# Kernel tuning notes

Hardware: AMD Instinct MI355X
Metric: run time of the kernel (lower is better)

Reference implementation:

```python
import jax, jax.numpy as jnp
import numpy as np

N = 16384
C = 4        # in_channels
K = 16       # neighbors
H = 64       # mlp width


def setup_inputs() -> dict:
    key = jax.random.key(0)
    k0, k1, k2, k3, k4 = jax.random.split(key, 5)
    x = jax.random.normal(k0, (N, C), dtype=jnp.float32)
    # nn.Linear(2C, 64) and nn.Linear(64, 64): weight [out, in], bias [out]
    W1 = jax.random.normal(k1, (H, 2 * C), dtype=jnp.float32) * (1.0 / np.sqrt(2 * C))
    b1 = jax.random.normal(k2, (H,), dtype=jnp.float32) * 0.01
    W2 = jax.random.normal(k3, (H, H), dtype=jnp.float32) * (1.0 / np.sqrt(H))
    b2 = jax.random.normal(k4, (H,), dtype=jnp.float32) * 0.01
    return {"x": x, "W1": W1, "b1": b1, "W2": W2, "b2": b2}


def reference(x, W1, b1, W2, b2):
    # x: [N, C] single point cloud (torch code unsqueezes batch dim 0)
    xs = jax.lax.stop_gradient(x)  # knn indices computed under no_grad
    # pairwise = -||xi - xj||^2 = 2*xi.xj - ||xi||^2 - ||xj||^2
    xx = jnp.sum(xs * xs, axis=1)                      # [N]
    pairwise = 2.0 * (xs @ xs.T) - xx[:, None] - xx[None, :]  # [N, N]
    _, idx = jax.lax.top_k(pairwise, K)                # [N, K] (self included, dist 0 is max)
    neigh = x[idx]                                     # [N, K, C] gather
    center = jnp.broadcast_to(x[:, None, :], (x.shape[0], K, C))
    edge = jnp.concatenate([neigh - center, center], axis=-1)  # [N, K, 2C]
    h = jax.nn.relu(jnp.einsum('nkc,hc->nkh', edge, W1) + b1)
    h = jax.nn.relu(jnp.einsum('nkh,gh->nkg', h, W2) + b2)     # [N, K, H]
    out = jnp.mean(h, axis=1)                          # [N, H]
    return out[None]                                   # [1, N, H] matches torch output
```

## Files before the change

### kernel.cpp

```cpp
#include <hip/hip_runtime.h>
#include <math.h>

#define N_PTS 16384
#define K_NBR 16
#define H_DIM 64
#define TS    512
#define CAP   144

typedef unsigned long long u64;
typedef float v2f __attribute__((ext_vector_type(2)));

__device__ __forceinline__ int prefix_lt(u64 m) {
    return __builtin_amdgcn_mbcnt_hi((unsigned)(m >> 32),
           __builtin_amdgcn_mbcnt_lo((unsigned)m, 0));
}
__device__ __forceinline__ u64 mkkey(unsigned vbits, unsigned idx) {
    unsigned of = vbits ^ (unsigned)(((int)vbits >> 31) | 0x80000000);
    return ((u64)of << 32) | (unsigned)(~idx);
}
__device__ __forceinline__ unsigned keyidx(u64 k) { return ~(unsigned)k; }

__device__ __forceinline__ float readlane_f(float v, int l) {
    return __uint_as_float(__builtin_amdgcn_readlane(__float_as_uint(v), l));
}

__device__ __forceinline__ float wave_sort_f32(float v, int lane) {
#pragma unroll
    for (int k = 2; k <= 64; k <<= 1) {
#pragma unroll
        for (int j = k >> 1; j > 0; j >>= 1) {
            float o = __shfl_xor(v, j, 64);
            bool keep_min = (((lane & k) == 0) == ((lane & j) == 0));
            v = keep_min ? fminf(v, o) : fmaxf(v, o);
        }
    }
    return v;
}
__device__ __forceinline__ u64 wave_sort_u64(u64 v, int lane) {
#pragma unroll
    for (int k = 2; k <= 64; k <<= 1) {
#pragma unroll
        for (int j = k >> 1; j > 0; j >>= 1) {
            u64 o = __shfl_xor((unsigned long long)v, j, 64);
            bool keep_min = (((lane & k) == 0) == ((lane & j) == 0));
            u64 mn = (v < o) ? v : o;
            u64 mx = (v < o) ? o : v;
            v = keep_min ? mn : mx;
        }
    }
    return v;
}

__device__ __forceinline__ int wave_compact(uint2* buf, int cnt, float* tau,
                                            int lane) {
    float lm = -INFINITY;
    for (int s = lane; s < cnt; s += 64)
        lm = fmaxf(lm, __uint_as_float(buf[s].x));
    const float tv = readlane_f(wave_sort_f32(lm, lane), 48);
    int nc = 0;
    for (int s0 = 0; s0 < cnt; s0 += 64) {
        const int s = s0 + lane;
        uint2 e = make_uint2(0u, 0u);
        bool keep = false;
        if (s < cnt) { e = buf[s]; keep = (__uint_as_float(e.x) >= tv); }
        const u64 km = __ballot(keep);
        if (keep) buf[nc + prefix_lt(km)] = e;
        nc += (int)__popcll(km);
    }
    *tau = tv;
    return nc;
}

__global__ __launch_bounds__(256) void xx_kernel(const float4* __restrict__ x4,
                                                 float* __restrict__ xx) {
    int i = blockIdx.x * 256 + threadIdx.x;
    float4 v = x4[i];
    {
#pragma clang fp contract(off)
        float s0 = v.x * v.x;
        float s1 = v.y * v.y;
        float s2 = v.z * v.z;
        float s3 = v.w * v.w;
        xx[i] = ((s0 + s1) + s2) + s3;
    }
}

__global__ __launch_bounds__(256, 8) void knn_kernel(
        const float4* __restrict__ x4,
        const float* __restrict__ xx,
        int* __restrict__ knn) {
    __shared__ float xsc[4][TS];
    __shared__ float nxxs[TS];
    __shared__ uint2 buf[8][CAP];
    const int lane = threadIdx.x & 63;
    const int wave = threadIdx.x >> 6;
    const int row0 = blockIdx.x * 8 + wave * 2;

    float4 y[2]; float nxxi[2];
    uint2* bufr[2];
#pragma unroll
    for (int r = 0; r < 2; ++r) {
        const float4 t0 = x4[row0 + r];
        y[r] = make_float4(2.0f * t0.x, 2.0f * t0.y, 2.0f * t0.z, 2.0f * t0.w);
        nxxi[r] = -xx[row0 + r];
        bufr[r] = &buf[wave * 2 + r][0];
    }
    float tau[2]; int cnt[2];

    auto pair_p = [&](int e, int r) -> v2f {
        const v2f ax = *(const v2f*)&xsc[0][e];
        const v2f ay = *(const v2f*)&xsc[1][e];
        const v2f az = *(const v2f*)&xsc[2][e];
        const v2f aw = *(const v2f*)&xsc[3][e];
        const v2f nx = *(const v2f*)&nxxs[e];
        v2f acc = nx + (v2f){nxxi[r], nxxi[r]};
        acc = __builtin_elementwise_fma(ax, (v2f){y[r].x, y[r].x}, acc);
        acc = __builtin_elementwise_fma(ay, (v2f){y[r].y, y[r].y}, acc);
        acc = __builtin_elementwise_fma(az, (v2f){y[r].z, y[r].z}, acc);
        acc = __builtin_elementwise_fma(aw, (v2f){y[r].w, y[r].w}, acc);
        return acc;
    };

    for (int i = threadIdx.x; i < TS; i += 256) {
        const float4 v = x4[i];
        xsc[0][i] = v.x; xsc[1][i] = v.y; xsc[2][i] = v.z; xsc[3][i] = v.w;
        nxxs[i] = -xx[i];
    }
    __syncthreads();

    {
        const int e = 2 * lane;
#pragma unroll
        for (int r = 0; r < 2; ++r) {
            const v2f pp = pair_p(e, r);
            const float mx = fmaxf(pp.x, pp.y);
            tau[r] = readlane_f(wave_sort_f32(mx, lane), 48);
            const u64 ma = __ballot(pp.x >= tau[r]);
            const u64 mb = __ballot(pp.y >= tau[r]);
            const int ca = (int)__popcll(ma);
            if (pp.x >= tau[r])
                bufr[r][prefix_lt(ma)] =
                    make_uint2(__float_as_uint(pp.x), (unsigned)e);
            if (pp.y >= tau[r])
                bufr[r][ca + prefix_lt(mb)] =
                    make_uint2(__float_as_uint(pp.y), (unsigned)(e + 1));
            cnt[r] = ca + (int)__popcll(mb);
        }
    }

    auto do_iter = [&](int cbase) {
        const int e = (cbase & (TS - 1)) + 2 * lane;
        v2f pp[2]; u64 mm[2];
#pragma unroll
        for (int r = 0; r < 2; ++r) {
            pp[r] = pair_p(e, r);
            mm[r] = __ballot(fmaxf(pp[r].x, pp[r].y) > tau[r]);
        }
        if (mm[0] | mm[1]) {
#pragma unroll
            for (int r = 0; r < 2; ++r) {
                if (mm[r]) {
                    u64 ma = __ballot(pp[r].x > tau[r]);
                    u64 mb = __ballot(pp[r].y > tau[r]);
                    int add = (int)__popcll(ma) + (int)__popcll(mb);
                    if (cnt[r] + add > CAP) {
                        cnt[r] = wave_compact(bufr[r], cnt[r], &tau[r], lane);
                        ma = __ballot(pp[r].x > tau[r]);
                        mb = __ballot(pp[r].y > tau[r]);
                        add = (int)__popcll(ma) + (int)__popcll(mb);
                    }
                    const int ca = (int)__popcll(ma);
                    if (pp[r].x > tau[r])
                        bufr[r][cnt[r] + prefix_lt(ma)] =
                            make_uint2(__float_as_uint(pp[r].x),
                                       (unsigned)(cbase + 2 * lane));
                    if (pp[r].y > tau[r])
                        bufr[r][cnt[r] + ca + prefix_lt(mb)] =
                            make_uint2(__float_as_uint(pp[r].y),
                                       (unsigned)(cbase + 2 * lane + 1));
                    cnt[r] += add;
                }
            }
        }
    };

#pragma unroll
    for (int j = 1; j < TS / 128; ++j) do_iter(j * 128);

    for (int t = 1; t < N_PTS / TS; ++t) {
        const int base = t * TS;
        __syncthreads();
        for (int i = threadIdx.x; i < TS; i += 256) {
            const float4 v = x4[base + i];
            xsc[0][i] = v.x; xsc[1][i] = v.y; xsc[2][i] = v.z; xsc[3][i] = v.w;
            nxxs[i] = -xx[base + i];
        }
        __syncthreads();
#pragma unroll
        for (int j = 0; j < TS / 128; ++j) do_iter(base + j * 128);
    }

#pragma unroll
    for (int r = 0; r < 2; ++r) {
        const int c2 = wave_compact(bufr[r], cnt[r], &tau[r], lane);
        u64 key = 0;
        if (lane < c2) {
            const uint2 e = bufr[r][lane];
            key = mkkey(e.x, e.y);
        }
        key = wave_sort_u64(key, lane);
        if (lane >= 48)
            knn[(row0 + r) * K_NBR + (lane - 48)] = (int)keyidx(key);
    }
}

__global__ __launch_bounds__(256, 2) void mlp_kernel(
        const float4* __restrict__ x4,
        const int* __restrict__ knn,
        const float4* __restrict__ W2f4,
        const float* __restrict__ W1,
        const float* __restrict__ b1,
        const float* __restrict__ b2,
        float* __restrict__ out) {
    __shared__ __align__(16) float4 w2s[16][64];
    __shared__ __align__(16) float  h1s[4][32][68];
    __shared__ __align__(16) float4 xjs[4][32];
    const int lane = threadIdx.x & 63;
    const int wave = threadIdx.x >> 6;
    const int kq   = lane >> 4;
    const int gp   = lane & 15;
    const int p0   = (blockIdx.x * 4 + wave) * 2;

    for (int q = threadIdx.x; q < 1024; q += 256)
        w2s[q & 15][q >> 4] = W2f4[q];
    __syncthreads();

    float w1r[8];
#pragma unroll
    for (int c = 0; c < 8; ++c) w1r[c] = W1[lane * 8 + c];
    const float b1r = b1[lane];
    float b2r[4];
#pragma unroll
    for (int gq = 0; gq < 4; ++gq) b2r[gq] = b2[gq * 16 + gp];

    if (lane < 32) {
        const int pp = lane >> 4;
        const int nb = knn[(p0 + pp) * K_NBR + (lane & 15)];
        xjs[wave][lane] = x4[nb];
    }

#pragma unroll
    for (int pp = 0; pp < 2; ++pp) {
        const float4 xi = x4[p0 + pp];
        float hb = b1r;
        hb = fmaf(w1r[4] - w1r[0], xi.x, hb);
        hb = fmaf(w1r[5] - w1r[1], xi.y, hb);
        hb = fmaf(w1r[6] - w1r[2], xi.z, hb);
        hb = fmaf(w1r[7] - w1r[3], xi.w, hb);
#pragma unroll
        for (int k = 0; k < K_NBR; ++k) {
            const float4 xj = xjs[wave][pp * 16 + k];
            float h = hb;
            h = fmaf(w1r[0], xj.x, h);
            h = fmaf(w1r[1], xj.y, h);
            h = fmaf(w1r[2], xj.z, h);
            h = fmaf(w1r[3], xj.w, h);
            h1s[wave][pp * 16 + k][lane] = fmaxf(h, 0.0f);
        }
    }

    v2f acc[2][4][4];
#pragma unroll
    for (int pp = 0; pp < 2; ++pp)
#pragma unroll
        for (int kk = 0; kk < 4; ++kk)
#pragma unroll
            for (int gq = 0; gq < 4; ++gq)
                acc[pp][kk][gq] = (v2f){b2r[gq], 0.0f};

#pragma unroll
    for (int h4 = 0; h4 < 16; ++h4) {
        float4 w4[4];
#pragma unroll
        for (int gq = 0; gq < 4; ++gq) w4[gq] = w2s[h4][gq * 16 + gp];
#pragma unroll
        for (int pp = 0; pp < 2; ++pp) {
#pragma unroll
            for (int kk = 0; kk < 4; ++kk) {
                const float4 hv =
                    *(const float4*)&h1s[wave][pp * 16 + kq * 4 + kk][h4 * 4];
#pragma unroll
                for (int gq = 0; gq < 4; ++gq) {
                    acc[pp][kk][gq] = __builtin_elementwise_fma(
                        (v2f){hv.x, hv.y}, (v2f){w4[gq].x, w4[gq].y},
                        acc[pp][kk][gq]);
                    acc[pp][kk][gq] = __builtin_elementwise_fma(
                        (v2f){hv.z, hv.w}, (v2f){w4[gq].z, w4[gq].w},
                        acc[pp][kk][gq]);
                }
            }
        }
    }

#pragma unroll
    for (int pp = 0; pp < 2; ++pp) {
        float s[4];
#pragma unroll
        for (int gq = 0; gq < 4; ++gq) {
            s[gq] = 0.0f;
#pragma unroll
            for (int kk = 0; kk < 4; ++kk) {
                const float v = acc[pp][kk][gq].x + acc[pp][kk][gq].y;
                s[gq] += fmaxf(v, 0.0f);
            }
        }
#pragma unroll
        for (int off = 16; off <= 32; off <<= 1)
#pragma unroll
            for (int gq = 0; gq < 4; ++gq)
                s[gq] += __shfl_xor(s[gq], off, 64);

        out[(p0 + pp) * H_DIM + kq * 16 + gp] = s[kq] * (1.0f / 16.0f);
    }
}

extern "C" void kernel_launch(void* const* d_in, const int* in_sizes, int n_in,
                              void* d_out, int out_size, void* d_ws, size_t ws_size,
                              hipStream_t stream) {
    (void)in_sizes; (void)n_in; (void)out_size; (void)ws_size;
    const float* x  = (const float*)d_in[0];
    const float* W1 = (const float*)d_in[1];
    const float* b1 = (const float*)d_in[2];
    const float* W2 = (const float*)d_in[3];
    const float* b2 = (const float*)d_in[4];
    float* out = (float*)d_out;

    float* xx  = (float*)d_ws;
    int*   knn = (int*)((char*)d_ws + N_PTS * sizeof(float));

    const float4* x4 = (const float4*)x;

    xx_kernel <<<N_PTS / 256, 256, 0, stream>>>(x4, xx);
    knn_kernel<<<N_PTS / 8,   256, 0, stream>>>(x4, xx, knn);
    mlp_kernel<<<N_PTS / 8,   256, 0, stream>>>(
        x4, knn, (const float4*)W2, W1, b1, b2, out);
}
```

Measured before the change: 216.4 us.

## Compute kNN pairwise scores with split-bf16 MFMA and per-row candidate buffers

The kNN distance computation moves from scalar packed-FMA over shared-memory tiles to MFMA 16x16x32 bf16 instructions. The fp32 coordinates and norms are split into three bf16 parts (hi/mid/lo) by a prep kernel so the products approximate fp32 precision. Each wave now handles 16 rows using MFMA output tiles, with per-row candidate buffers and a threshold seeded from a first pass. Launch geometry changes to 64 rows per block at one block per SM. This aims to replace the FMA-bound score evaluation with matrix-core throughput, at the risk of rounding differences that could reorder near-tied neighbours and lower occupancy.

```diff
diff --git a/kernel.cpp b/kernel.cpp
--- a/kernel.cpp
+++ b/kernel.cpp
@@ -4,16 +4,15 @@
 #define N_PTS 16384
 #define K_NBR 16
 #define H_DIM 64
-#define TS    512
-#define CAP   144
+#define CAP   120
+#define NBLK  (N_PTS / 16)
 
 typedef unsigned long long u64;
-typedef float v2f __attribute__((ext_vector_type(2)));
-
-__device__ __forceinline__ int prefix_lt(u64 m) {
-    return __builtin_amdgcn_mbcnt_hi((unsigned)(m >> 32),
-           __builtin_amdgcn_mbcnt_lo((unsigned)m, 0));
-}
+typedef unsigned short u16;
+typedef float v2f   __attribute__((ext_vector_type(2)));
+typedef float f32x4 __attribute__((ext_vector_type(4)));
+typedef short bf16x8 __attribute__((ext_vector_type(8)));
+
 __device__ __forceinline__ u64 mkkey(unsigned vbits, unsigned idx) {
     unsigned of = vbits ^ (unsigned)(((int)vbits >> 31) | 0x80000000);
     return ((u64)of << 32) | (unsigned)(~idx);
@@ -22,6 +21,14 @@
 
 __device__ __forceinline__ float readlane_f(float v, int l) {
     return __uint_as_float(__builtin_amdgcn_readlane(__float_as_uint(v), l));
+}
+
+__device__ __forceinline__ u16 f2bf(float f) {
+    unsigned u = __float_as_uint(f);
+    return (u16)((u + 0x7FFFu + ((u >> 16) & 1u)) >> 16);
+}
+__device__ __forceinline__ float bf2f(u16 b) {
+    return __uint_as_float(((unsigned)b) << 16);
 }
 
 __device__ __forceinline__ float wave_sort_f32(float v, int lane) {
@@ -51,8 +58,9 @@
     return v;
 }
 
-__device__ __forceinline__ int wave_compact(uint2* buf, int cnt, float* tau,
-                                            int lane) {
+struct CompRes { int nc; float tau; };
+__device__ __attribute__((noinline)) CompRes wave_compact(uint2* buf, int cnt,
+                                                          int lane) {
     float lm = -INFINITY;
     for (int s = lane; s < cnt; s += 64)
         lm = fmaxf(lm, __uint_as_float(buf[s].x));
@@ -64,153 +72,249 @@
         bool keep = false;
         if (s < cnt) { e = buf[s]; keep = (__uint_as_float(e.x) >= tv); }
         const u64 km = __ballot(keep);
-        if (keep) buf[nc + prefix_lt(km)] = e;
+        if (keep) {
+            int pfx = (int)__popcll(km & ((1ull << lane) - 1));
+            buf[nc + pfx] = e;
+        }
         nc += (int)__popcll(km);
     }
-    *tau = tv;
-    return nc;
-}
-
-__global__ __launch_bounds__(256) void xx_kernel(const float4* __restrict__ x4,
-                                                 float* __restrict__ xx) {
-    int i = blockIdx.x * 256 + threadIdx.x;
-    float4 v = x4[i];
+    CompRes r; r.nc = nc; r.tau = tv;
+    return r;
+}
+
+__global__ __launch_bounds__(256) void prep_kernel(const float4* __restrict__ x4,
+                                                   u16* __restrict__ bf) {
+    const int i = blockIdx.x * 256 + threadIdx.x;
+    const float4 v = x4[i];
+    float xx;
     {
 #pragma clang fp contract(off)
-        float s0 = v.x * v.x;
-        float s1 = v.y * v.y;
-        float s2 = v.z * v.z;
-        float s3 = v.w * v.w;
-        xx[i] = ((s0 + s1) + s2) + s3;
-    }
-}
-
-__global__ __launch_bounds__(256, 8) void knn_kernel(
+        float s0 = v.x * v.x, s1 = v.y * v.y, s2 = v.z * v.z, s3 = v.w * v.w;
+        xx = ((s0 + s1) + s2) + s3;
+    }
+    float c[4] = {v.x, v.y, v.z, v.w};
+    u16 H[4], M[4], L[4];
+#pragma unroll
+    for (int q = 0; q < 4; ++q) {
+        float f = c[q];
+        u16 h = f2bf(f);            float fh = bf2f(h);
+        u16 m = f2bf(f - fh);       float fm = bf2f(m);
+        u16 l = f2bf(f - fh - fm);
+        H[q] = h; M[q] = m; L[q] = l;
+    }
+    const float nx = -xx;
+    u16 X0 = f2bf(nx);              float x0f = bf2f(X0);
+    u16 X1 = f2bf(nx - x0f);        float x1f = bf2f(X1);
+    u16 X2 = f2bf(nx - x0f - x1f);
+    u16 o[32];
+#pragma unroll
+    for (int q = 0; q < 4; ++q) {
+        o[q]      = H[q];
+        o[4 + q]  = M[q];
+        o[8 + q]  = H[q];
+        o[12 + q] = L[q];
+        o[16 + q] = H[q];
+        o[20 + q] = M[q];
+    }
+    o[24] = X0; o[25] = X1; o[26] = X2;
+    o[27] = 0; o[28] = 0; o[29] = 0; o[30] = 0; o[31] = 0;
+    uint4* dst = (uint4*)(bf + (size_t)i * 32);
+#pragma unroll
+    for (int q2 = 0; q2 < 4; ++q2) {
+        uint4 w;
+        w.x = (unsigned)o[q2 * 8 + 0] | ((unsigned)o[q2 * 8 + 1] << 16);
+        w.y = (unsigned)o[q2 * 8 + 2] | ((unsigned)o[q2 * 8 + 3] << 16);
+        w.z = (unsigned)o[q2 * 8 + 4] | ((unsigned)o[q2 * 8 + 5] << 16);
+        w.w = (unsigned)o[q2 * 8 + 6] | ((unsigned)o[q2 * 8 + 7] << 16);
+        dst[q2] = w;
+    }
+}
+
+__global__ __launch_bounds__(256, 1) void knn_kernel(
         const float4* __restrict__ x4,
-        const float* __restrict__ xx,
+        const u16* __restrict__ bfrag,
         int* __restrict__ knn) {
-    __shared__ float xsc[4][TS];
-    __shared__ float nxxs[TS];
-    __shared__ uint2 buf[8][CAP];
+    __shared__ __align__(16) uint2 buf[4][16][CAP];
     const int lane = threadIdx.x & 63;
     const int wave = threadIdx.x >> 6;
-    const int row0 = blockIdx.x * 8 + wave * 2;
-
-    float4 y[2]; float nxxi[2];
-    uint2* bufr[2];
-#pragma unroll
-    for (int r = 0; r < 2; ++r) {
-        const float4 t0 = x4[row0 + r];
-        y[r] = make_float4(2.0f * t0.x, 2.0f * t0.y, 2.0f * t0.z, 2.0f * t0.w);
-        nxxi[r] = -xx[row0 + r];
-        bufr[r] = &buf[wave * 2 + r][0];
-    }
-    float tau[2]; int cnt[2];
-
-    auto pair_p = [&](int e, int r) -> v2f {
-        const v2f ax = *(const v2f*)&xsc[0][e];
-        const v2f ay = *(const v2f*)&xsc[1][e];
-        const v2f az = *(const v2f*)&xsc[2][e];
-        const v2f aw = *(const v2f*)&xsc[3][e];
-        const v2f nx = *(const v2f*)&nxxs[e];
-        v2f acc = nx + (v2f){nxxi[r], nxxi[r]};
-        acc = __builtin_elementwise_fma(ax, (v2f){y[r].x, y[r].x}, acc);
-        acc = __builtin_elementwise_fma(ay, (v2f){y[r].y, y[r].y}, acc);
-        acc = __builtin_elementwise_fma(az, (v2f){y[r].z, y[r].z}, acc);
-        acc = __builtin_elementwise_fma(aw, (v2f){y[r].w, y[r].w}, acc);
-        return acc;
+    const int g    = lane >> 4;
+    const int rowbase = blockIdx.x * 64 + wave * 16;
+
+    const float4 xi = x4[rowbase + (lane & 15)];
+    u16 Ha[4], Ma[4], La[4];
+    {
+        float yy[4] = {2.f * xi.x, 2.f * xi.y, 2.f * xi.z, 2.f * xi.w};
+#pragma unroll
+        for (int q = 0; q < 4; ++q) {
+            u16 h = f2bf(yy[q]);             float fh = bf2f(h);
+            u16 m = f2bf(yy[q] - fh);        float fm = bf2f(m);
+            u16 l = f2bf(yy[q] - fh - fm);
+            Ha[q] = h; Ma[q] = m; La[q] = l;
+        }
+    }
+    bf16x8 afrag;
+    {
+        const u16 ONEB = 0x3F80;
+#pragma unroll
+        for (int q = 0; q < 4; ++q) {
+            u16 lo, hi;
+            if (g == 0)      { lo = Ha[q]; hi = Ha[q]; }
+            else if (g == 1) { lo = Ma[q]; hi = Ha[q]; }
+            else if (g == 2) { lo = La[q]; hi = Ma[q]; }
+            else             { lo = (q < 3) ? ONEB : 0; hi = 0; }
+            afrag[q]     = (short)lo;
+            afrag[q + 4] = (short)hi;
+        }
+    }
+    const f32x4 zacc = {0.f, 0.f, 0.f, 0.f};
+    const bf16x8* bp = (const bf16x8*)bfrag + ((lane & 15) * 4 + g);
+    const u64 gmask  = 0xFFFFull << (g * 16);
+    const u64 gbelow = ((1ull << lane) - 1) & gmask;
+
+    float tau0, tau1, tau2, tau3;
+    {
+        float mx0 = -INFINITY, mx1 = -INFINITY, mx2 = -INFINITY, mx3 = -INFINITY;
+        bf16x8 P[4];
+#pragma unroll
+        for (int i = 0; i < 4; ++i) P[i] = bp[i * 64];
+        for (int t = 0; t < 32; t += 4) {
+            bf16x8 Pn[4];
+#pragma unroll
+            for (int i = 0; i < 4; ++i) {
+                int tp = t + 4 + i; if (tp > 31) tp = 31;
+                Pn[i] = bp[tp * 64];
+            }
+            f32x4 aa[4];
+#pragma unroll
+            for (int i = 0; i < 4; ++i)
+                aa[i] = __builtin_amdgcn_mfma_f32_16x16x32_bf16(afrag, P[i],
+                                                                zacc, 0, 0, 0);
+#pragma unroll
+            for (int i = 0; i < 4; ++i) {
+                mx0 = fmaxf(mx0, aa[i][0]);
+                mx1 = fmaxf(mx1, aa[i][1]);
+                mx2 = fmaxf(mx2, aa[i][2]);
+                mx3 = fmaxf(mx3, aa[i][3]);
+            }
+#pragma unroll
+            for (int i = 0; i < 4; ++i) P[i] = Pn[i];
+        }
+#pragma unroll
+        for (int off = 1; off < 16; off <<= 1) {
+            mx0 = fminf(mx0, __shfl_xor(mx0, off, 64));
+            mx1 = fminf(mx1, __shfl_xor(mx1, off, 64));
+            mx2 = fminf(mx2, __shfl_xor(mx2, off, 64));
+            mx3 = fminf(mx3, __shfl_xor(mx3, off, 64));
+        }
+        tau0 = mx0; tau1 = mx1; tau2 = mx2; tau3 = mx3;
+    }
+
+    unsigned c0 = 0, c1 = 0, c2 = 0, c3 = 0;
+
+    auto insert_body = [&](f32x4 av, int colbase, bool ge) {
+        const unsigned colidx = (unsigned)(colbase + (lane & 15));
+        while (true) {
+            const bool h0 = ge ? (av[0] >= tau0) : (av[0] > tau0);
+            const bool h1 = ge ? (av[1] >= tau1) : (av[1] > tau1);
+            const bool h2 = ge ? (av[2] >= tau2) : (av[2] > tau2);
+            const bool h3 = ge ? (av[3] >= tau3) : (av[3] > tau3);
+            const u64 m0 = __ballot(h0), m1 = __ballot(h1);
+            const u64 m2 = __ballot(h2), m3 = __ballot(h3);
+            const unsigned gc0 = (unsigned)__popcll(m0 & gmask);
+            const unsigned gc1 = (unsigned)__popcll(m1 & gmask);
+            const unsigned gc2 = (unsigned)__popcll(m2 & gmask);
+            const unsigned gc3 = (unsigned)__popcll(m3 & gmask);
+            const bool ov = (c0 + gc0 > CAP) || (c1 + gc1 > CAP) ||
+                            (c2 + gc2 > CAP) || (c3 + gc3 > CAP);
+            if (!__ballot(ov)) {
+                if (m0) { const unsigned pos = c0 + (unsigned)__popcll(m0 & gbelow);
+                    if (h0) buf[wave][g * 4 + 0][pos] =
+                        make_uint2(__float_as_uint(av[0]), colidx); }
+                if (m1) { const unsigned pos = c1 + (unsigned)__popcll(m1 & gbelow);
+                    if (h1) buf[wave][g * 4 + 1][pos] =
+                        make_uint2(__float_as_uint(av[1]), colidx); }
+                if (m2) { const unsigned pos = c2 + (unsigned)__popcll(m2 & gbelow);
+                    if (h2) buf[wave][g * 4 + 2][pos] =
+                        make_uint2(__float_as_uint(av[2]), colidx); }
+                if (m3) { const unsigned pos = c3 + (unsigned)__popcll(m3 & gbelow);
+                    if (h3) buf[wave][g * 4 + 3][pos] =
+                        make_uint2(__float_as_uint(av[3]), colidx); }
+                c0 += gc0; c1 += gc1; c2 += gc2; c3 += gc3;
+                return;
+            }
+            for (int r = 0; r < 16; ++r) {
+                const int srcl = (r >> 2) * 16;
+                const int jj = r & 3;
+                unsigned cr;
+                if (jj == 0)      cr = __builtin_amdgcn_readlane(c0, srcl);
+                else if (jj == 1) cr = __builtin_amdgcn_readlane(c1, srcl);
+                else if (jj == 2) cr = __builtin_amdgcn_readlane(c2, srcl);
+                else              cr = __builtin_amdgcn_readlane(c3, srcl);
+                if (cr + 16u > CAP) {
+                    CompRes res = wave_compact(&buf[wave][r][0], (int)cr, lane);
+                    if ((lane >> 4) == (r >> 2)) {
+                        if (jj == 0)      { c0 = (unsigned)res.nc; tau0 = fmaxf(tau0, res.tau); }
+                        else if (jj == 1) { c1 = (unsigned)res.nc; tau1 = fmaxf(tau1, res.tau); }
+                        else if (jj == 2) { c2 = (unsigned)res.nc; tau2 = fmaxf(tau2, res.tau); }
+                        else              { c3 = (unsigned)res.nc; tau3 = fmaxf(tau3, res.tau); }
+                    }
+                }
+            }
+        }
     };
 
-    for (int i = threadIdx.x; i < TS; i += 256) {
-        const float4 v = x4[i];
-        xsc[0][i] = v.x; xsc[1][i] = v.y; xsc[2][i] = v.z; xsc[3][i] = v.w;
-        nxxs[i] = -xx[i];
-    }
-    __syncthreads();
-
-    {
-        const int e = 2 * lane;
-#pragma unroll
-        for (int r = 0; r < 2; ++r) {
-            const v2f pp = pair_p(e, r);
-            const float mx = fmaxf(pp.x, pp.y);
-            tau[r] = readlane_f(wave_sort_f32(mx, lane), 48);
-            const u64 ma = __ballot(pp.x >= tau[r]);
-            const u64 mb = __ballot(pp.y >= tau[r]);
-            const int ca = (int)__popcll(ma);
-            if (pp.x >= tau[r])
-                bufr[r][prefix_lt(ma)] =
-                    make_uint2(__float_as_uint(pp.x), (unsigned)e);
-            if (pp.y >= tau[r])
-                bufr[r][ca + prefix_lt(mb)] =
-                    make_uint2(__float_as_uint(pp.y), (unsigned)(e + 1));
-            cnt[r] = ca + (int)__popcll(mb);
-        }
-    }
-
-    auto do_iter = [&](int cbase) {
-        const int e = (cbase & (TS - 1)) + 2 * lane;
-        v2f pp[2]; u64 mm[2];
-#pragma unroll
-        for (int r = 0; r < 2; ++r) {
-            pp[r] = pair_p(e, r);
-            mm[r] = __ballot(fmaxf(pp[r].x, pp[r].y) > tau[r]);
-        }
-        if (mm[0] | mm[1]) {
-#pragma unroll
-            for (int r = 0; r < 2; ++r) {
-                if (mm[r]) {
-                    u64 ma = __ballot(pp[r].x > tau[r]);
-                    u64 mb = __ballot(pp[r].y > tau[r]);
-                    int add = (int)__popcll(ma) + (int)__popcll(mb);
-                    if (cnt[r] + add > CAP) {
-                        cnt[r] = wave_compact(bufr[r], cnt[r], &tau[r], lane);
-                        ma = __ballot(pp[r].x > tau[r]);
-                        mb = __ballot(pp[r].y > tau[r]);
-                        add = (int)__popcll(ma) + (int)__popcll(mb);
-                    }
-                    const int ca = (int)__popcll(ma);
-                    if (pp[r].x > tau[r])
-                        bufr[r][cnt[r] + prefix_lt(ma)] =
-                            make_uint2(__float_as_uint(pp[r].x),
-                                       (unsigned)(cbase + 2 * lane));
-                    if (pp[r].y > tau[r])
-                        bufr[r][cnt[r] + ca + prefix_lt(mb)] =
-                            make_uint2(__float_as_uint(pp[r].y),
-                                       (unsigned)(cbase + 2 * lane + 1));
-                    cnt[r] += add;
-                }
-            }
-        }
-    };
-
-#pragma unroll
-    for (int j = 1; j < TS / 128; ++j) do_iter(j * 128);
-
-    for (int t = 1; t < N_PTS / TS; ++t) {
-        const int base = t * TS;
-        __syncthreads();
-        for (int i = threadIdx.x; i < TS; i += 256) {
-            const float4 v = x4[base + i];
-            xsc[0][i] = v.x; xsc[1][i] = v.y; xsc[2][i] = v.z; xsc[3][i] = v.w;
-            nxxs[i] = -xx[base + i];
-        }
-        __syncthreads();
-#pragma unroll
-        for (int j = 0; j < TS / 128; ++j) do_iter(base + j * 128);
-    }
-
-#pragma unroll
-    for (int r = 0; r < 2; ++r) {
-        const int c2 = wave_compact(bufr[r], cnt[r], &tau[r], lane);
+#define RANGE_LOOP(T0, T1, GEC)  do {                                        \
+    bf16x8 Bc[8], Bn[8];                                                     \
+    _Pragma("unroll")                                                        \
+    for (int i = 0; i < 8; ++i) Bc[i] = bp[((T0) + i) * 64];                 \
+    for (int t = (T0); t < (T1); t += 8) {                                   \
+        _Pragma("unroll")                                                    \
+        for (int i = 0; i < 8; ++i) {                                        \
+            int tp = t + 8 + i; if (tp >= (T1)) tp = (T1) - 1;               \
+            Bn[i] = bp[tp * 64];                                             \
+        }                                                                    \
+        f32x4 A8[8];                                                         \
+        _Pragma("unroll")                                                    \
+        for (int i = 0; i < 8; ++i)                                          \
+            A8[i] = __builtin_amdgcn_mfma_f32_16x16x32_bf16(afrag, Bc[i],    \
+                                                            zacc, 0, 0, 0);  \
+        _Pragma("unroll")                                                    \
+        for (int i = 0; i < 8; ++i) {                                        \
+            const f32x4 av = A8[i];                                          \
+            bool h0 = GEC ? (av[0] >= tau0) : (av[0] > tau0);                \
+            bool h1 = GEC ? (av[1] >= tau1) : (av[1] > tau1);                \
+            bool h2 = GEC ? (av[2] >= tau2) : (av[2] > tau2);                \
+            bool h3 = GEC ? (av[3] >= tau3) : (av[3] > tau3);                \
+            if (__ballot(h0) | __ballot(h1) | __ballot(h2) | __ballot(h3))   \
+                insert_body(av, (t + i) * 16, GEC);                          \
+        }                                                                    \
+        _Pragma("unroll")                                                    \
+        for (int i = 0; i < 8; ++i) Bc[i] = Bn[i];                           \
+    }                                                                        \
+} while (0)
+
+    RANGE_LOOP(0, 32, true);
+    RANGE_LOOP(32, NBLK, false);
+
+#undef RANGE_LOOP
+
+#pragma unroll 1
+    for (int r = 0; r < 16; ++r) {
+        const int srcl = (r >> 2) * 16;
+        const int jj = r & 3;
+        unsigned cru;
+        if (jj == 0)      cru = __builtin_amdgcn_readlane(c0, srcl);
+        else if (jj == 1) cru = __builtin_amdgcn_readlane(c1, srcl);
+        else if (jj == 2) cru = __builtin_amdgcn_readlane(c2, srcl);
+        else              cru = __builtin_amdgcn_readlane(c3, srcl);
+        int c = (int)cru;
+        uint2* br = &buf[wave][r][0];
+        if (c > 64) { CompRes res = wave_compact(br, c, lane); c = res.nc; }
         u64 key = 0;
-        if (lane < c2) {
-            const uint2 e = bufr[r][lane];
-            key = mkkey(e.x, e.y);
-        }
+        if (lane < c) { const uint2 e = br[lane]; key = mkkey(e.x, e.y); }
         key = wave_sort_u64(key, lane);
         if (lane >= 48)
-            knn[(row0 + r) * K_NBR + (lane - 48)] = (int)keyidx(key);
+            knn[(rowbase + r) * K_NBR + (lane - 48)] = (int)keyidx(key);
     }
 }
 
@@ -335,13 +439,13 @@
     const float* b2 = (const float*)d_in[4];
     float* out = (float*)d_out;
 
-    float* xx  = (float*)d_ws;
-    int*   knn = (int*)((char*)d_ws + N_PTS * sizeof(float));
+    int* knn   = (int*)d_ws;
+    u16* bfrag = (u16*)((char*)d_ws + (size_t)N_PTS * K_NBR * sizeof(int));
 
     const float4* x4 = (const float4*)x;
 
-    xx_kernel <<<N_PTS / 256, 256, 0, stream>>>(x4, xx);
-    knn_kernel<<<N_PTS / 8,   256, 0, stream>>>(x4, xx, knn);
-    mlp_kernel<<<N_PTS / 8,   256, 0, stream>>>(
+    prep_kernel<<<N_PTS / 256, 256, 0, stream>>>(x4, bfrag);
+    knn_kernel <<<N_PTS / 64,  256, 0, stream>>>(x4, bfrag, knn);
+    mlp_kernel <<<N_PTS / 8,   256, 0, stream>>>(
         x4, knn, (const float4*)W2, W1, b1, b2, out);
 }
```

Measured after the change: 596.8 us. +175.8%, slower.
